# Performance work log

Hardware: AMD Instinct MI355X
Metric: run time of the kernel (lower is better)

## Reference

```python
import jax, jax.numpy as jnp
import numpy as np

MC = 16384
N_STEPS = 120
PERIOD = 30
N_MAT = 4
N_STR = 21
WIDTH_DIFF = 50
WIDTH_VAN = 30
WIDTH_EXO = 20
N_HIDDEN = 3  # n_layers=4 -> input layer + 3 hidden layers + output layer
R = 0.05
TIMEGRID = jnp.asarray(np.linspace(0.0, 1.0, N_STEPS + 1).astype(np.float32))
STRIKES = jnp.asarray(np.linspace(0.8, 1.2, N_STR).astype(np.float32))


def _init_net(key, d_in, width, d_out):
    ks = jax.random.split(key, 6)
    f = lambda k, shape, fan: jax.random.normal(k, shape, jnp.float32) / np.sqrt(fan).astype(np.float32)
    return dict(
        W0=f(ks[0], (N_MAT, d_in, width), d_in),
        b0=f(ks[1], (N_MAT, width), width),
        hW=f(ks[2], (N_MAT, N_HIDDEN, width, width), width),
        hb=f(ks[3], (N_MAT, N_HIDDEN, width), width),
        Wo=f(ks[4], (N_MAT, width, d_out), width),
        bo=f(ks[5], (N_MAT, d_out), width),
    )


def setup_inputs() -> dict:
    key = jax.random.key(0)
    kz, kd, kv, ke = jax.random.split(key, 4)
    inp = {
        "S0": jnp.ones((1,), jnp.float32),
        "z": jax.random.normal(kz, (MC, N_STEPS), jnp.float32),
    }
    for name, net in (("d", _init_net(kd, 2, WIDTH_DIFF, 1)),
                      ("v", _init_net(kv, 2, WIDTH_VAN, N_STR * N_MAT)),
                      ("e", _init_net(ke, N_STEPS + 2, WIDTH_EXO, 1))):
        for pn, arr in net.items():
            inp[name + pn] = arr
    inp["MC_samples"] = MC
    inp["ind_T"] = N_STEPS
    inp["period_length"] = PERIOD
    return inp


def _mlp(x, W0, b0, hW, hb, Wo, bo, softplus_out):
    h = jax.nn.relu(x @ W0 + b0)
    for k in range(hW.shape[0]):  # static small number of hidden layers
        h = jax.nn.relu(h @ hW[k] + hb[k])
    y = h @ Wo + bo
    return jax.nn.softplus(y) if softplus_out else y


def _forward(S0, z, dW0, db0, dhW, dhb, dWo, dbo,
             vW0, vb0, vhW, vhb, vWo, vbo,
             eW0, eb0, ehW, ehb, eWo, ebo,
             MC_samples, ind_T, period_length, remat=False):
    sg = jax.lax.stop_gradient
    S_init = jnp.ones((MC_samples, 1), jnp.float32) * S0
    path0 = jnp.zeros((MC_samples, N_STEPS + 1), jnp.float32).at[:, 0].set(S_init[:, 0])
    zeros_mat = jnp.zeros((N_MAT, N_STR), jnp.float32)

    def step(carry, i):
        S_old, cv_v, cv_e, run_max, path, pv, pvv = carry
        idx = (i - 1) // period_length
        t0 = TIMEGRID[i - 1]
        h = TIMEGRID[i] - TIMEGRID[i - 1]
        sqh = jnp.sqrt(h)
        dWn = sqh * jax.lax.dynamic_slice_in_dim(z, i - 1, 1, 1)  # (MC,1)
        t = jnp.full_like(S_old, t0)
        diff = _mlp(jnp.concatenate([t, S_old], 1),
                    dW0[idx], db0[idx], dhW[idx], dhb[idx], dWo[idx], dbo[idx], True)
        Sd, diffd = sg(S_old), sg(diff)
        S_new = (S_old
                 + R * S_old * h / (1.0 + R * Sd * sqh)
                 + S_old * diff * dWn / (1.0 + Sd * diffd * sqh))
        disc = jnp.exp(-R * t0)
        cv_v = cv_v + disc * Sd * diffd * dWn * _mlp(
            jnp.concatenate([t, Sd], 1),
            vW0[idx], vb0[idx], vhW[idx], vhb[idx], vWo[idx], vbo[idx], False)
        cv_e = cv_e + disc * Sd * diffd * dWn * _mlp(
            jnp.concatenate([t, path], 1),
            eW0[idx], eb0[idx], ehW[idx], ehb[idx], eWo[idx], ebo[idx], False)
        path = jax.lax.dynamic_update_slice(path, sg(S_new), (0, i))
        run_max = jnp.maximum(run_max, S_new)
        # vanilla prices at maturities (i multiple of period_length)
        ind_m = i // period_length - 1
        disc_i = jnp.exp(-R * TIMEGRID[i])
        cv_row = jax.lax.dynamic_slice_in_dim(
            cv_v.reshape(MC_samples, N_MAT, N_STR), ind_m, 1, 1)[:, 0, :]
        pr = disc_i * jnp.maximum(S_new - STRIKES[None, :], 0.0) - cv_row  # (MC, N_STR)
        is_mat = (i % period_length) == 0
        pv = jnp.where(is_mat, jax.lax.dynamic_update_index_in_dim(pv, pr.mean(0), ind_m, 0), pv)
        pvv = jnp.where(is_mat, jax.lax.dynamic_update_index_in_dim(pvv, jnp.var(pr, axis=0, ddof=1), ind_m, 0), pvv)
        return (S_new, cv_v, cv_e, run_max, path, pv, pvv), None

    body = jax.checkpoint(step) if remat else step
    carry0 = (S_init,
              jnp.zeros((MC_samples, N_STR * N_MAT), jnp.float32),
              jnp.zeros((MC_samples, 1), jnp.float32),
              S_init, path0, zeros_mat, zeros_mat)
    (S_T, cv_v, cv_e, run_max, path, pv, pvv), _ = jax.lax.scan(
        body, carry0, jnp.arange(1, ind_T + 1))

    sgv = jax.lax.stop_gradient
    exotic = run_max - S_T
    discT = jnp.exp(-R * TIMEGRID[ind_T])
    e = discT * exotic
    error = sgv(e) - jnp.mean(sgv(e)) - sgv(cv_e)
    price_exo = e - cv_e
    return pv, pvv, price_exo, price_exo.mean(), jnp.var(price_exo, ddof=1), error


def reference(S0, z, dW0, db0, dhW, dhb, dWo, dbo,
              vW0, vb0, vhW, vhb, vWo, vbo,
              eW0, eb0, ehW, ehb, eWo, ebo,
              MC_samples, ind_T, period_length):
    return _forward(S0, z, dW0, db0, dhW, dhb, dWo, dbo,
                    vW0, vb0, vhW, vhb, vWo, vbo,
                    eW0, eb0, ehW, ehb, eWo, ebo,
                    MC_samples, ind_T, period_length)
```

## Files before the change

### kernel.cpp

```cpp
#include <hip/hip_runtime.h>
#include <math.h>

#define MC      16384
#define NSTEPS  120
#define PER     30
#define NMAT    4
#define NSTR    21
#define RRATE   0.05f
#define NBLK    512
#define NSAMP   32

typedef short short8  __attribute__((ext_vector_type(8)));
typedef short short4v __attribute__((ext_vector_type(4)));
typedef float f32x4   __attribute__((ext_vector_type(4)));

#define WS_PRPART 0
#define WS_EPART  (NMAT*NSTR*2*NBLK)
#define WS_MEANE  (WS_EPART + NBLK)

#define OUT_PV    0
#define OUT_PVV   84
#define OUT_PEXO  168
#define OUT_MEAN  16552
#define OUT_VAR   16553
#define OUT_ERR   16554

__device__ __forceinline__ float tgridf(int i)  { return (float)((double)i * (1.0/120.0)); }
__device__ __forceinline__ float strikef(int s) { return (float)(0.8 + (double)s * 0.02); }
__device__ __forceinline__ float softplusf(float x){
  return fmaxf(x, 0.0f) + log1pf(expf(-fabsf(x)));
}
__device__ __forceinline__ unsigned short f2bf(float f){
  unsigned u = __builtin_bit_cast(unsigned, f);
  unsigned r = (u + 0x7FFFu + ((u>>16)&1u)) >> 16;
  return (unsigned short)r;
}
__device__ __forceinline__ float bf2f(unsigned short u){
  return __builtin_bit_cast(float, ((unsigned)u)<<16);
}
__device__ __forceinline__ int swaddr(int row, int slot, int inner){
  return row*256 + (((slot + row) & 15) << 4) + inner;
}
__device__ __forceinline__ short8 rdA(const unsigned short* H, int mt, int base, int lane){
  int addr = swaddr(mt*16 + (lane&15), base + (lane>>4), 0);
  return *(const short8*)((const char*)H + addr);
}
__device__ __forceinline__ f32x4 mm(short8 a, short8 b, f32x4 c){
  return __builtin_amdgcn_mfma_f32_16x16x32_bf16(a, b, c, 0, 0, 0);
}
__device__ __forceinline__ void stD(unsigned short* H, int colbase, int mt, int lane,
                                    f32x4 acc, bool relu){
  int col  = colbase + (lane & 15);
  int slot = col >> 3, inner = (col & 7)*2;
  #pragma unroll
  for (int i2=0;i2<4;++i2){
    int rw = mt*16 + ((lane>>4)<<2) + i2;
    float v = acc[i2];
    if (relu) v = fmaxf(v, 0.0f);
    *(unsigned short*)((char*)H + swaddr(rw, slot, inner)) = f2bf(v);
  }
}
__device__ __forceinline__ short8 mkBd(const float* __restrict__ W, const float* __restrict__ bias,
                                       int n0, int kt, int lane){
  short8 r;
  int n = n0 + (lane&15);
  #pragma unroll
  for (int i2=0;i2<8;++i2){
    int k = kt*32 + ((lane>>4)<<3) + i2;
    float w;
    if (k<50)       w = (n<50)? W[k*50+n] : 0.f;
    else if (k==50) w = (n<50)? bias[n] : ((n==50)? 1.f : 0.f);
    else            w = 0.f;
    r[i2] = (short)f2bf(w);
  }
  return r;
}
__device__ __forceinline__ short8 mkBq(const float* __restrict__ W, const float* __restrict__ bias,
                                       int KV, int n0, int lane){
  short8 r;
  int n = n0 + (lane&15);
  #pragma unroll
  for (int i2=0;i2<8;++i2){
    int k = ((lane>>4)<<3) + i2;
    float w;
    if (k<KV)       w = (n<KV)? W[k*KV+n] : 0.f;
    else if (k==KV) w = (n<KV)? bias[n] : ((n==KV)? 1.f : 0.f);
    else            w = 0.f;
    r[i2] = (short)f2bf(w);
  }
  return r;
}

extern "C" __global__ void __launch_bounds__(256,2) mc_main(
    const float* __restrict__ S0p, const float* __restrict__ z,
    const float* __restrict__ dW0, const float* __restrict__ db0,
    const float* __restrict__ dhW, const float* __restrict__ dhb,
    const float* __restrict__ dWo, const float* __restrict__ dbo,
    const float* __restrict__ vW0, const float* __restrict__ vb0,
    const float* __restrict__ vhW, const float* __restrict__ vhb,
    const float* __restrict__ vWo, const float* __restrict__ vbo,
    const float* __restrict__ eW0, const float* __restrict__ eb0,
    const float* __restrict__ ehW, const float* __restrict__ ehb,
    const float* __restrict__ eWo, const float* __restrict__ ebo,
    float* __restrict__ out, float* __restrict__ ws)
{
  __shared__ unsigned short Hb0[NSAMP*128];
  __shared__ unsigned short Hb1[NSAMP*128];
  __shared__ short8 BqL[4][3][64];
  __shared__ short8 BdL[4][6][64];
  __shared__ float vh3f[NSAMP*40];
  __shared__ float zper[NSAMP*30];
  __shared__ float eW0per[NMAT*600];
  __shared__ float dW0s[128];
  __shared__ float db0s[64];
  __shared__ float vW0s[64];
  __shared__ float vb0s[32];
  __shared__ float eW0ts[20];
  __shared__ float eb0s[20];
  __shared__ float dWoL[64];
  __shared__ float eWoL[32];
  __shared__ float Sb[NSAMP], ebuf[NSAMP];
  __shared__ float part[2*84*2];

  const int tid  = threadIdx.x;
  const int lane = tid & 63;
  const int wid  = __builtin_amdgcn_readfirstlane(tid >> 6);
  const int blk  = blockIdx.x;
  const int r    = tid >> 3;
  const int cc   = tid & 7;

  const int  ntd = wid;
  const bool isv = (wid < 2);
  const int  ntq = wid & 1;

  const float S0v = S0p[0];
  float S = S0v, runmax = S0v, cvE = 0.f;
  f32x4 rr[3];
  #pragma unroll
  for (int q=0;q<3;++q){ rr[q][0]=0.f; rr[q][1]=0.f; rr[q][2]=0.f; rr[q][3]=0.f; }
  float aE[NMAT][4];
  #pragma unroll
  for (int mt2=0;mt2<NMAT;++mt2){ aE[mt2][0]=0.f; aE[mt2][1]=0.f; aE[mt2][2]=0.f; aE[mt2][3]=0.f; }
  float G_[4] = {0.f,0.f,0.f,0.f};

  #pragma unroll 1
  for (int p=0;p<NMAT;++p){
    for (int q=tid; q<NSAMP*30; q+=256){ int r2=q/30, c2=q%30; zper[q] = z[(size_t)(blk*NSAMP+r2)*NSTEPS + p*30 + c2]; }
    for (int q=tid; q<NMAT*600; q+=256){ int mat=q/600, k=q%600; eW0per[q] = eW0[mat*2440 + p*600 + 20 + k]; }
    if (tid < 128){
      int rw = tid>>6, j = tid&63;
      dW0s[tid] = (j<50)? dW0[p*100 + rw*50 + j] : 0.f;
    } else if (tid < 192){
      int j = tid-128;
      db0s[j] = (j<50)? db0[p*50+j] : ((j==50)? 1.f : 0.f);
    } else {
      int idx = tid-192, rw = idx>>5, j = idx&31;
      vW0s[idx] = (j<30)? vW0[p*60 + rw*30 + j] : 0.f;
    }
    if (tid < 32)       vb0s[tid] = (tid<30)? vb0[p*30+tid] : ((tid==30)? 1.f : 0.f);
    else if (tid < 52){ int j=tid-32; eW0ts[j]=eW0[p*2440+j]; eb0s[j]=eb0[p*20+j]; }
    else if (tid < 116){ int j=tid-52; dWoL[j] = (j<50)? dWo[p*50+j] : 0.f; }
    else if (tid < 148){ int j=tid-116; eWoL[j] = (j<20)? eWo[p*20+j] : 0.f; }

    const float dboS = dbo[p], eboS = ebo[p];

    const float* dhWp = dhW + p*7500;
    const float* dhbp = dhb + p*150;
    BdL[wid][0][lane] = mkBd(dhWp,      dhbp,     ntd*16, 0, lane);
    BdL[wid][1][lane] = mkBd(dhWp,      dhbp,     ntd*16, 1, lane);
    BdL[wid][2][lane] = mkBd(dhWp+2500, dhbp+50,  ntd*16, 0, lane);
    BdL[wid][3][lane] = mkBd(dhWp+2500, dhbp+50,  ntd*16, 1, lane);
    BdL[wid][4][lane] = mkBd(dhWp+5000, dhbp+100, ntd*16, 0, lane);
    BdL[wid][5][lane] = mkBd(dhWp+5000, dhbp+100, ntd*16, 1, lane);
    {
      const float* qW    = isv ? (vhW + p*2700) : (ehW + p*1200);
      const float* qb    = isv ? (vhb + p*90)   : (ehb + p*60);
      const int    qstep = isv ? 900 : 400;
      const int    qN    = isv ? 30  : 20;
      BqL[wid][0][lane] = mkBq(qW,         qb,        qN, ntq*16, lane);
      BqL[wid][1][lane] = mkBq(qW+qstep,   qb+qN,     qN, ntq*16, lane);
      BqL[wid][2][lane] = mkBq(qW+2*qstep, qb+2*qN,   qN, ntq*16, lane);
    }
    const int qbase = isv ? 8 : 12;
    const int qcolb = (isv?64:96) + ntq*16;

    __syncthreads();

    #pragma unroll 1
    for (int ii=1; ii<=PER; ++ii){
      const float t0  = tgridf(p*PER + ii - 1);
      const float t1  = tgridf(p*PER + ii);
      const float h   = t1 - t0;
      const float sqh = sqrtf(h);

      {
        short8 hv;
        #pragma unroll
        for (int k=0;k<8;++k){
          int j = cc*8 + k;
          float u = fmaxf(fmaf(t0, dW0s[j], fmaf(S, dW0s[64+j], db0s[j])), 0.f);
          hv[k] = (short)f2bf(u);
        }
        *(short8*)((char*)Hb0 + swaddr(r, cc, 0)) = hv;
        short4v vv;
        #pragma unroll
        for (int k=0;k<4;++k){
          int j = cc*4 + k;
          float u = fmaxf(fmaf(t0, vW0s[j], fmaf(S, vW0s[32+j], vb0s[j])), 0.f);
          vv[k] = (short)f2bf(u);
        }
        *(short4v*)((char*)Hb0 + swaddr(r, 8+(cc>>1), (cc&1)*8)) = vv;
        short4v ev = {0,0,0,0};
        if (cc < 5){
          const int o = (ii-1)*20 + cc*4;
          f32x4 w0 = *(const f32x4*)&eW0per[        o];
          f32x4 w1 = *(const f32x4*)&eW0per[ 600 +  o];
          f32x4 w2 = *(const f32x4*)&eW0per[1200 +  o];
          f32x4 w3 = *(const f32x4*)&eW0per[1800 +  o];
          #pragma unroll
          for (int k=0;k<4;++k){
            aE[0][k] = fmaf(S, w0[k], aE[0][k]);
            aE[1][k] = fmaf(S, w1[k], aE[1][k]);
            aE[2][k] = fmaf(S, w2[k], aE[2][k]);
            aE[3][k] = fmaf(S, w3[k], aE[3][k]);
            float a = (p==0)?aE[0][k]:(p==1)?aE[1][k]:(p==2)?aE[2][k]:aE[3][k];
            int j = cc*4 + k;
            float e0 = fmaxf(t0*eW0ts[j] + a + eb0s[j], 0.f);
            ev[k] = (short)f2bf(e0);
          }
        } else if (cc == 5){
          ev[0] = (short)0x3F80;
        }
        *(short4v*)((char*)Hb0 + swaddr(r, 12+(cc>>1), (cc&1)*8)) = ev;
      }
      __syncthreads();
      {
        short8 b0 = BdL[wid][0][lane], b1 = BdL[wid][1][lane];
        short8 a00=rdA(Hb0,0,0,lane), a01=rdA(Hb0,0,4,lane);
        short8 a10=rdA(Hb0,1,0,lane), a11=rdA(Hb0,1,4,lane);
        f32x4 c0={0.f,0.f,0.f,0.f}, c1={0.f,0.f,0.f,0.f};
        c0=mm(a00,b0,c0); c0=mm(a01,b1,c0);
        c1=mm(a10,b0,c1); c1=mm(a11,b1,c1);
        stD(Hb1, ntd*16, 0, lane, c0, true);
        stD(Hb1, ntd*16, 1, lane, c1, true);
        short8 Bq = BqL[wid][0][lane];
        short8 q0=rdA(Hb0,0,qbase,lane), q1=rdA(Hb0,1,qbase,lane);
        f32x4 cq0={0.f,0.f,0.f,0.f}, cq1={0.f,0.f,0.f,0.f};
        cq0=mm(q0,Bq,cq0); cq1=mm(q1,Bq,cq1);
        stD(Hb1, qcolb, 0, lane, cq0, true);
        stD(Hb1, qcolb, 1, lane, cq1, true);
      }
      __syncthreads();
      {
        short8 b0 = BdL[wid][2][lane], b1 = BdL[wid][3][lane];
        short8 a00=rdA(Hb1,0,0,lane), a01=rdA(Hb1,0,4,lane);
        short8 a10=rdA(Hb1,1,0,lane), a11=rdA(Hb1,1,4,lane);
        f32x4 c0={0.f,0.f,0.f,0.f}, c1={0.f,0.f,0.f,0.f};
        c0=mm(a00,b0,c0); c0=mm(a01,b1,c0);
        c1=mm(a10,b0,c1); c1=mm(a11,b1,c1);
        stD(Hb0, ntd*16, 0, lane, c0, true);
        stD(Hb0, ntd*16, 1, lane, c1, true);
        short8 Bq = BqL[wid][1][lane];
        short8 q0=rdA(Hb1,0,qbase,lane), q1=rdA(Hb1,1,qbase,lane);
        f32x4 cq0={0.f,0.f,0.f,0.f}, cq1={0.f,0.f,0.f,0.f};
        cq0=mm(q0,Bq,cq0); cq1=mm(q1,Bq,cq1);
        stD(Hb0, qcolb, 0, lane, cq0, true);
        stD(Hb0, qcolb, 1, lane, cq1, true);
      }
      __syncthreads();
      {
        short8 b0 = BdL[wid][4][lane], b1 = BdL[wid][5][lane];
        short8 a00=rdA(Hb0,0,0,lane), a01=rdA(Hb0,0,4,lane);
        short8 a10=rdA(Hb0,1,0,lane), a11=rdA(Hb0,1,4,lane);
        f32x4 c0={0.f,0.f,0.f,0.f}, c1={0.f,0.f,0.f,0.f};
        c0=mm(a00,b0,c0); c0=mm(a01,b1,c0);
        c1=mm(a10,b0,c1); c1=mm(a11,b1,c1);
        stD(Hb1, ntd*16, 0, lane, c0, true);
        stD(Hb1, ntd*16, 1, lane, c1, true);
        short8 Bq = BqL[wid][2][lane];
        short8 q0=rdA(Hb0,0,qbase,lane), q1=rdA(Hb0,1,qbase,lane);
        f32x4 cq0={0.f,0.f,0.f,0.f}, cq1={0.f,0.f,0.f,0.f};
        cq0=mm(q0,Bq,cq0); cq1=mm(q1,Bq,cq1);
        if (isv){
          #pragma unroll
          for (int i2=0;i2<4;++i2){
            int r0 = ((lane>>4)<<2) + i2;
            vh3f[ r0     *40 + ntq*16 + (lane&15)] = fmaxf(cq0[i2], 0.f);
            vh3f[(16+r0) *40 + ntq*16 + (lane&15)] = fmaxf(cq1[i2], 0.f);
          }
        } else {
          stD(Hb1, qcolb, 0, lane, cq0, true);
          stD(Hb1, qcolb, 1, lane, cq1, true);
        }
      }
      __syncthreads();
      {
        float yp = 0.f;
        {
          short8 hv = *(const short8*)((const char*)Hb1 + swaddr(r, cc, 0));
          #pragma unroll
          for (int k=0;k<8;++k) yp = fmaf(bf2f((unsigned short)hv[k]), dWoL[cc*8+k], yp);
        }
        float yep = 0.f;
        if (cc < 5){
          short4v hv = *(const short4v*)((const char*)Hb1 + swaddr(r, 12+(cc>>1), (cc&1)*8));
          #pragma unroll
          for (int k=0;k<4;++k) yep = fmaf(bf2f((unsigned short)hv[k]), eWoL[cc*4+k], yep);
        }
        #pragma unroll
        for (int mk=1; mk<8; mk<<=1){ yp += __shfl_xor(yp, mk); yep += __shfl_xor(yep, mk); }
        const float y    = yp + dboS;
        const float diff = softplusf(y);
        const float zv   = zper[r*30 + (ii-1)];
        const float dWn  = sqh * zv;
        const float d1 = 1.f + RRATE*S*sqh;
        const float d2 = 1.f + S*diff*sqh;
        const float Snew = S + RRATE*S*h/d1 + S*diff*dWn/d2;
        const float disc = expf(-RRATE*t0);
        const float coef = disc * S * diff * dWn;
        cvE = fmaf(coef, yep + eboS, cvE);
        runmax = fmaxf(runmax, Snew);
        {
          f32x4 vv = *(const f32x4*)&vh3f[r*40 + cc*4];
          #pragma unroll
          for (int k=0;k<4;++k) G_[k] = fmaf(coef, vv[k], G_[k]);
        }
        S = Snew;

        if (ii==PER){
          short4v gv;
          #pragma unroll
          for (int k=0;k<4;++k){ gv[k] = (short)f2bf(G_[k]); G_[k] = 0.f; }
          *(short4v*)((char*)Hb0 + swaddr(r, cc>>1, (cc&1)*8)) = gv;
          if (cc==0) Sb[r] = S;
        }
      }

      if (ii==PER){
        __syncthreads();
        const float disc_i = expf(-RRATE*t1);
        const float* vWop = vWo + p*2520;
        const float* vbop = vbo + p*84;
        #pragma unroll
        for (int q3=0;q3<3;++q3){
          const int T = wid*3 + q3;
          const int mtr = T/6, ntr = T%6;
          short8 a = rdA(Hb0, mtr, 0, lane);
          const int col = ntr*16 + (lane&15);
          short8 bw;
          #pragma unroll
          for (int i2=0;i2<8;++i2){
            int k = ((lane>>4)<<3)+i2;
            float w = 0.f;
            if (col < 84){
              if (k < 30)       w = vWop[k*84+col];
              else if (k == 30) w = vbop[col];
            }
            bw[i2] = (short)f2bf(w);
          }
          f32x4 d4 = {0.f,0.f,0.f,0.f};
          d4 = mm(a,bw,d4);
          const int s = col - p*NSTR;
          const bool inr = (s>=0) && (s<NSTR) && (col<84);
          const float K = strikef(s);
          float ssum=0.f, ssq=0.f;
          #pragma unroll
          for (int i2=0;i2<4;++i2){
            int row = mtr*16 + ((lane>>4)<<2) + i2;
            rr[q3][i2] += d4[i2];
            if (inr){
              float pr = disc_i*fmaxf(Sb[row]-K,0.f) - rr[q3][i2];
              ssum += pr; ssq = fmaf(pr,pr,ssq);
            }
          }
          ssum += __shfl_down(ssum,16); ssum += __shfl_down(ssum,32);
          ssq  += __shfl_down(ssq ,16); ssq  += __shfl_down(ssq ,32);
          if (inr && lane<16){
            part[(mtr*84+col)*2+0] = ssum;
            part[(mtr*84+col)*2+1] = ssq;
          }
        }
        __syncthreads();
        if (tid < NSTR){
          int cidx = p*NSTR + tid;
          ws[WS_PRPART + (cidx*2+0)*NBLK + blk] = part[cidx*2] + part[(84+cidx)*2];
        } else if (tid >= 64 && tid < 64+NSTR){
          int cidx = p*NSTR + (tid-64);
          ws[WS_PRPART + (cidx*2+1)*NBLK + blk] = part[cidx*2+1] + part[(84+cidx)*2+1];
        }
        __syncthreads();
      }
    }
  }

  if (cc==0){
    const float discT = expf(-RRATE);
    const float e = discT * (runmax - S);
    out[OUT_PEXO + blk*NSAMP + r] = e - cvE;
    ebuf[r] = e;
  }
  __syncthreads();
  if (tid < 32){
    float se = ebuf[tid];
    se += __shfl_down(se,16); se += __shfl_down(se,8);
    se += __shfl_down(se,4);  se += __shfl_down(se,2); se += __shfl_down(se,1);
    if (tid==0) ws[WS_EPART + blk] = se;
  }
}

extern "C" __global__ void fin_pv(const float* __restrict__ ws, float* __restrict__ out){
  const int t = threadIdx.x;
  if (t >= NMAT*NSTR) return;
  float sum=0.0f, ssq=0.0f;
  for (int b=0;b<NBLK;++b){
    sum += ws[WS_PRPART + (t*2+0)*NBLK + b];
    ssq += ws[WS_PRPART + (t*2+1)*NBLK + b];
  }
  out[OUT_PV  + t] = sum * (1.0f/MC);
  out[OUT_PVV + t] = (ssq - sum*sum*(1.0f/MC)) * (1.0f/(MC-1));
}

extern "C" __global__ void fin_pe(float* out, float* ws){
  __shared__ float sA[4], sB[4], sC[4];
  const int t = threadIdx.x;
  float sum=0.0f, ssq=0.0f;
  for (int idx=t; idx<MC; idx+=256){
    const float v = out[OUT_PEXO+idx];
    sum += v; ssq = fmaf(v,v,ssq);
  }
  float es = ws[WS_EPART + t] + ws[WS_EPART + 256 + t];
  for (int o=32;o>0;o>>=1){
    sum += __shfl_down(sum,o);
    ssq += __shfl_down(ssq,o);
    es  += __shfl_down(es,o);
  }
  const int w=t>>6, lane=t&63;
  if (lane==0){ sA[w]=sum; sB[w]=ssq; sC[w]=es; }
  __syncthreads();
  if (t==0){
    const float s=sA[0]+sA[1]+sA[2]+sA[3];
    const float q=sB[0]+sB[1]+sB[2]+sB[3];
    const float e=sC[0]+sC[1]+sC[2]+sC[3];
    out[OUT_MEAN]=s*(1.0f/MC);
    out[OUT_VAR]=(q - s*s*(1.0f/MC))*(1.0f/(MC-1));
    ws[WS_MEANE]=e*(1.0f/MC);
  }
}

extern "C" __global__ void fin_err(float* out, const float* __restrict__ ws){
  const int m = blockIdx.x*blockDim.x + threadIdx.x;
  if (m < MC) out[OUT_ERR+m] = out[OUT_PEXO+m] - ws[WS_MEANE];
}

extern "C" void kernel_launch(void* const* d_in, const int* in_sizes, int n_in,
                              void* d_out, int out_size, void* d_ws, size_t ws_size,
                              hipStream_t stream){
  (void)in_sizes; (void)n_in; (void)out_size; (void)ws_size;
  const float* S0 =(const float*)d_in[0];
  const float* z  =(const float*)d_in[1];
  const float* dW0=(const float*)d_in[2];
  const float* db0=(const float*)d_in[3];
  const float* dhW=(const float*)d_in[4];
  const float* dhb=(const float*)d_in[5];
  const float* dWo=(const float*)d_in[6];
  const float* dbo=(const float*)d_in[7];
  const float* vW0=(const float*)d_in[8];
  const float* vb0=(const float*)d_in[9];
  const float* vhW=(const float*)d_in[10];
  const float* vhb=(const float*)d_in[11];
  const float* vWo=(const float*)d_in[12];
  const float* vbo=(const float*)d_in[13];
  const float* eW0=(const float*)d_in[14];
  const float* eb0=(const float*)d_in[15];
  const float* ehW=(const float*)d_in[16];
  const float* ehb=(const float*)d_in[17];
  const float* eWo=(const float*)d_in[18];
  const float* ebo=(const float*)d_in[19];
  float* out=(float*)d_out;
  float* ws =(float*)d_ws;

  mc_main<<<dim3(NBLK),dim3(256),0,stream>>>(S0,z,dW0,db0,dhW,dhb,dWo,dbo,
                                             vW0,vb0,vhW,vhb,vWo,vbo,
                                             eW0,eb0,ehW,ehb,eWo,ebo,out,ws);
  fin_pv <<<dim3(1), dim3(128),0,stream>>>(ws,out);
  fin_pe <<<dim3(1), dim3(256),0,stream>>>(out,ws);
  fin_err<<<dim3(64),dim3(256),0,stream>>>(out,ws);
}
```

Before: 467.7 us.

## Give each wavefront its own 8-sample tile to eliminate per-layer block barriers

Result: slower. 587.3 us (+25.6%).

```diff
diff --git a/kernel.cpp b/kernel.cpp
--- a/kernel.cpp
+++ b/kernel.cpp
@@ -16,7 +16,7 @@
 
 #define WS_PRPART 0
 #define WS_EPART  (NMAT*NSTR*2*NBLK)
-#define WS_MEANE  (WS_EPART + NBLK)
+#define WS_MEANE  (WS_EPART + 2048)
 
 #define OUT_PV    0
 #define OUT_PVV   84
@@ -89,6 +89,34 @@
     r[i2] = (short)f2bf(w);
   }
   return r;
+}
+__device__ __forceinline__ void layer_all(const unsigned short* src, unsigned short* dst,
+                                          const short8 (*__restrict__ Bd)[64],
+                                          const short8 (*__restrict__ Bv)[64],
+                                          const short8 (*__restrict__ Be)[64],
+                                          int l, int lane){
+  short8 a0 = rdA(src,0,0,lane), a1 = rdA(src,0,4,lane);
+  short8 av = rdA(src,0,8,lane);
+  short8 ae = rdA(src,0,12,lane);
+  #pragma unroll
+  for (int nt=0;nt<4;++nt){
+    f32x4 c={0.f,0.f,0.f,0.f};
+    c = mm(a0, Bd[l*8+nt*2  ][lane], c);
+    c = mm(a1, Bd[l*8+nt*2+1][lane], c);
+    stD(dst, nt*16, 0, lane, c, true);
+  }
+  #pragma unroll
+  for (int nt=0;nt<2;++nt){
+    f32x4 c={0.f,0.f,0.f,0.f};
+    c = mm(av, Bv[l*2+nt][lane], c);
+    stD(dst, 64+nt*16, 0, lane, c, true);
+  }
+  #pragma unroll
+  for (int nt=0;nt<2;++nt){
+    f32x4 c={0.f,0.f,0.f,0.f};
+    c = mm(ae, Be[l*2+nt][lane], c);
+    stD(dst, 96+nt*16, 0, lane, c, true);
+  }
 }
 
 extern "C" __global__ void __launch_bounds__(256,2) mc_main(
@@ -104,87 +132,70 @@
     const float* __restrict__ eWo, const float* __restrict__ ebo,
     float* __restrict__ out, float* __restrict__ ws)
 {
-  __shared__ unsigned short Hb0[NSAMP*128];
-  __shared__ unsigned short Hb1[NSAMP*128];
-  __shared__ short8 BqL[4][3][64];
-  __shared__ short8 BdL[4][6][64];
-  __shared__ float vh3f[NSAMP*40];
+  __shared__ unsigned short tiles[4][2][2048];
+  __shared__ short8 BdA[24][64];
+  __shared__ short8 BvA[6][64];
+  __shared__ short8 BeA[6][64];
+  __shared__ unsigned short eW0b[2400];
   __shared__ float zper[NSAMP*30];
-  __shared__ float eW0per[NMAT*600];
-  __shared__ float dW0s[128];
-  __shared__ float db0s[64];
-  __shared__ float vW0s[64];
-  __shared__ float vb0s[32];
-  __shared__ float eW0ts[20];
-  __shared__ float eb0s[20];
-  __shared__ float dWoL[64];
-  __shared__ float eWoL[32];
-  __shared__ float Sb[NSAMP], ebuf[NSAMP];
-  __shared__ float part[2*84*2];
+  __shared__ float dW0s[128], db0s[64], vW0s[64], vb0s[32];
+  __shared__ float eW0ts[20], eb0s[20], dWoL[64], eWoL[32];
+  __shared__ float SbW[32];
 
   const int tid  = threadIdx.x;
   const int lane = tid & 63;
   const int wid  = __builtin_amdgcn_readfirstlane(tid >> 6);
   const int blk  = blockIdx.x;
-  const int r    = tid >> 3;
-  const int cc   = tid & 7;
-
-  const int  ntd = wid;
-  const bool isv = (wid < 2);
-  const int  ntq = wid & 1;
+  const int s    = lane >> 3;
+  const int c8   = lane & 7;
+
+  unsigned short* T0 = &tiles[wid][0][0];
+  unsigned short* T1 = &tiles[wid][1][0];
+
+  for (int q=tid; q<4*2*2048; q+=256) ((unsigned short*)tiles)[q] = 0;
 
   const float S0v = S0p[0];
   float S = S0v, runmax = S0v, cvE = 0.f;
-  f32x4 rr[3];
-  #pragma unroll
-  for (int q=0;q<3;++q){ rr[q][0]=0.f; rr[q][1]=0.f; rr[q][2]=0.f; rr[q][3]=0.f; }
   float aE[NMAT][4];
   #pragma unroll
-  for (int mt2=0;mt2<NMAT;++mt2){ aE[mt2][0]=0.f; aE[mt2][1]=0.f; aE[mt2][2]=0.f; aE[mt2][3]=0.f; }
+  for (int m2=0;m2<NMAT;++m2){ aE[m2][0]=0.f; aE[m2][1]=0.f; aE[m2][2]=0.f; aE[m2][3]=0.f; }
   float G_[4] = {0.f,0.f,0.f,0.f};
+  f32x4 rr[6];
+  #pragma unroll
+  for (int q=0;q<6;++q){ rr[q][0]=0.f; rr[q][1]=0.f; rr[q][2]=0.f; rr[q][3]=0.f; }
 
   #pragma unroll 1
   for (int p=0;p<NMAT;++p){
+    __syncthreads();
     for (int q=tid; q<NSAMP*30; q+=256){ int r2=q/30, c2=q%30; zper[q] = z[(size_t)(blk*NSAMP+r2)*NSTEPS + p*30 + c2]; }
-    for (int q=tid; q<NMAT*600; q+=256){ int mat=q/600, k=q%600; eW0per[q] = eW0[mat*2440 + p*600 + 20 + k]; }
-    if (tid < 128){
-      int rw = tid>>6, j = tid&63;
-      dW0s[tid] = (j<50)? dW0[p*100 + rw*50 + j] : 0.f;
-    } else if (tid < 192){
-      int j = tid-128;
-      db0s[j] = (j<50)? db0[p*50+j] : ((j==50)? 1.f : 0.f);
-    } else {
-      int idx = tid-192, rw = idx>>5, j = idx&31;
-      vW0s[idx] = (j<30)? vW0[p*60 + rw*30 + j] : 0.f;
-    }
+    for (int q=tid; q<2400; q+=256){ int mat=q/600, k=q%600; eW0b[q] = f2bf(eW0[mat*2440 + p*600 + 20 + k]); }
+    if (tid < 128){ int rw=tid>>6, j=tid&63; dW0s[tid] = (j<50)? dW0[p*100+rw*50+j] : 0.f; }
+    else if (tid < 192){ int j=tid-128; db0s[j] = (j<50)? db0[p*50+j] : ((j==50)? 1.f : 0.f); }
+    else { int idx=tid-192, rw=idx>>5, j=idx&31; vW0s[idx] = (j<30)? vW0[p*60+rw*30+j] : 0.f; }
     if (tid < 32)       vb0s[tid] = (tid<30)? vb0[p*30+tid] : ((tid==30)? 1.f : 0.f);
     else if (tid < 52){ int j=tid-32; eW0ts[j]=eW0[p*2440+j]; eb0s[j]=eb0[p*20+j]; }
     else if (tid < 116){ int j=tid-52; dWoL[j] = (j<50)? dWo[p*50+j] : 0.f; }
     else if (tid < 148){ int j=tid-116; eWoL[j] = (j<20)? eWo[p*20+j] : 0.f; }
+    {
+      const float* dhWp = dhW + p*7500; const float* dhbp = dhb + p*150;
+      const float* vhWp = vhW + p*2700; const float* vhbp = vhb + p*90;
+      const float* ehWp = ehW + p*1200; const float* ehbp = ehb + p*60;
+      for (int fid = wid; fid < 36; fid += 4){
+        if (fid < 24){
+          int l = fid>>3, nt = (fid>>1)&3, kt = fid&1;
+          BdA[fid][lane] = mkBd(dhWp + l*2500, dhbp + l*50, nt*16, kt, lane);
+        } else if (fid < 30){
+          int q = fid-24, l = q>>1, nt = q&1;
+          BvA[q][lane] = mkBq(vhWp + l*900, vhbp + l*30, 30, nt*16, lane);
+        } else {
+          int q = fid-30, l = q>>1, nt = q&1;
+          BeA[q][lane] = mkBq(ehWp + l*400, ehbp + l*20, 20, nt*16, lane);
+        }
+      }
+    }
+    __syncthreads();
 
     const float dboS = dbo[p], eboS = ebo[p];
-
-    const float* dhWp = dhW + p*7500;
-    const float* dhbp = dhb + p*150;
-    BdL[wid][0][lane] = mkBd(dhWp,      dhbp,     ntd*16, 0, lane);
-    BdL[wid][1][lane] = mkBd(dhWp,      dhbp,     ntd*16, 1, lane);
-    BdL[wid][2][lane] = mkBd(dhWp+2500, dhbp+50,  ntd*16, 0, lane);
-    BdL[wid][3][lane] = mkBd(dhWp+2500, dhbp+50,  ntd*16, 1, lane);
-    BdL[wid][4][lane] = mkBd(dhWp+5000, dhbp+100, ntd*16, 0, lane);
-    BdL[wid][5][lane] = mkBd(dhWp+5000, dhbp+100, ntd*16, 1, lane);
-    {
-      const float* qW    = isv ? (vhW + p*2700) : (ehW + p*1200);
-      const float* qb    = isv ? (vhb + p*90)   : (ehb + p*60);
-      const int    qstep = isv ? 900 : 400;
-      const int    qN    = isv ? 30  : 20;
-      BqL[wid][0][lane] = mkBq(qW,         qb,        qN, ntq*16, lane);
-      BqL[wid][1][lane] = mkBq(qW+qstep,   qb+qN,     qN, ntq*16, lane);
-      BqL[wid][2][lane] = mkBq(qW+2*qstep, qb+2*qN,   qN, ntq*16, lane);
-    }
-    const int qbase = isv ? 8 : 12;
-    const int qcolb = (isv?64:96) + ntq*16;
-
-    __syncthreads();
 
     #pragma unroll 1
     for (int ii=1; ii<=PER; ++ii){
@@ -197,121 +208,63 @@
         short8 hv;
         #pragma unroll
         for (int k=0;k<8;++k){
-          int j = cc*8 + k;
+          int j = c8*8 + k;
           float u = fmaxf(fmaf(t0, dW0s[j], fmaf(S, dW0s[64+j], db0s[j])), 0.f);
           hv[k] = (short)f2bf(u);
         }
-        *(short8*)((char*)Hb0 + swaddr(r, cc, 0)) = hv;
+        *(short8*)((char*)T0 + swaddr(s, c8, 0)) = hv;
         short4v vv;
         #pragma unroll
         for (int k=0;k<4;++k){
-          int j = cc*4 + k;
+          int j = c8*4 + k;
           float u = fmaxf(fmaf(t0, vW0s[j], fmaf(S, vW0s[32+j], vb0s[j])), 0.f);
           vv[k] = (short)f2bf(u);
         }
-        *(short4v*)((char*)Hb0 + swaddr(r, 8+(cc>>1), (cc&1)*8)) = vv;
+        *(short4v*)((char*)T0 + swaddr(s, 8+(c8>>1), (c8&1)*8)) = vv;
         short4v ev = {0,0,0,0};
-        if (cc < 5){
-          const int o = (ii-1)*20 + cc*4;
-          f32x4 w0 = *(const f32x4*)&eW0per[        o];
-          f32x4 w1 = *(const f32x4*)&eW0per[ 600 +  o];
-          f32x4 w2 = *(const f32x4*)&eW0per[1200 +  o];
-          f32x4 w3 = *(const f32x4*)&eW0per[1800 +  o];
+        if (c8 < 5){
+          const int o = (ii-1)*20 + c8*4;
           #pragma unroll
           for (int k=0;k<4;++k){
-            aE[0][k] = fmaf(S, w0[k], aE[0][k]);
-            aE[1][k] = fmaf(S, w1[k], aE[1][k]);
-            aE[2][k] = fmaf(S, w2[k], aE[2][k]);
-            aE[3][k] = fmaf(S, w3[k], aE[3][k]);
+            float w0 = bf2f(eW0b[      o+k]);
+            float w1 = bf2f(eW0b[ 600+ o+k]);
+            float w2 = bf2f(eW0b[1200+ o+k]);
+            float w3 = bf2f(eW0b[1800+ o+k]);
+            aE[0][k] = fmaf(S, w0, aE[0][k]);
+            aE[1][k] = fmaf(S, w1, aE[1][k]);
+            aE[2][k] = fmaf(S, w2, aE[2][k]);
+            aE[3][k] = fmaf(S, w3, aE[3][k]);
             float a = (p==0)?aE[0][k]:(p==1)?aE[1][k]:(p==2)?aE[2][k]:aE[3][k];
-            int j = cc*4 + k;
+            int j = c8*4 + k;
             float e0 = fmaxf(t0*eW0ts[j] + a + eb0s[j], 0.f);
             ev[k] = (short)f2bf(e0);
           }
-        } else if (cc == 5){
+        } else if (c8 == 5){
           ev[0] = (short)0x3F80;
         }
-        *(short4v*)((char*)Hb0 + swaddr(r, 12+(cc>>1), (cc&1)*8)) = ev;
+        *(short4v*)((char*)T0 + swaddr(s, 12+(c8>>1), (c8&1)*8)) = ev;
       }
-      __syncthreads();
-      {
-        short8 b0 = BdL[wid][0][lane], b1 = BdL[wid][1][lane];
-        short8 a00=rdA(Hb0,0,0,lane), a01=rdA(Hb0,0,4,lane);
-        short8 a10=rdA(Hb0,1,0,lane), a11=rdA(Hb0,1,4,lane);
-        f32x4 c0={0.f,0.f,0.f,0.f}, c1={0.f,0.f,0.f,0.f};
-        c0=mm(a00,b0,c0); c0=mm(a01,b1,c0);
-        c1=mm(a10,b0,c1); c1=mm(a11,b1,c1);
-        stD(Hb1, ntd*16, 0, lane, c0, true);
-        stD(Hb1, ntd*16, 1, lane, c1, true);
-        short8 Bq = BqL[wid][0][lane];
-        short8 q0=rdA(Hb0,0,qbase,lane), q1=rdA(Hb0,1,qbase,lane);
-        f32x4 cq0={0.f,0.f,0.f,0.f}, cq1={0.f,0.f,0.f,0.f};
-        cq0=mm(q0,Bq,cq0); cq1=mm(q1,Bq,cq1);
-        stD(Hb1, qcolb, 0, lane, cq0, true);
-        stD(Hb1, qcolb, 1, lane, cq1, true);
-      }
-      __syncthreads();
-      {
-        short8 b0 = BdL[wid][2][lane], b1 = BdL[wid][3][lane];
-        short8 a00=rdA(Hb1,0,0,lane), a01=rdA(Hb1,0,4,lane);
-        short8 a10=rdA(Hb1,1,0,lane), a11=rdA(Hb1,1,4,lane);
-        f32x4 c0={0.f,0.f,0.f,0.f}, c1={0.f,0.f,0.f,0.f};
-        c0=mm(a00,b0,c0); c0=mm(a01,b1,c0);
-        c1=mm(a10,b0,c1); c1=mm(a11,b1,c1);
-        stD(Hb0, ntd*16, 0, lane, c0, true);
-        stD(Hb0, ntd*16, 1, lane, c1, true);
-        short8 Bq = BqL[wid][1][lane];
-        short8 q0=rdA(Hb1,0,qbase,lane), q1=rdA(Hb1,1,qbase,lane);
-        f32x4 cq0={0.f,0.f,0.f,0.f}, cq1={0.f,0.f,0.f,0.f};
-        cq0=mm(q0,Bq,cq0); cq1=mm(q1,Bq,cq1);
-        stD(Hb0, qcolb, 0, lane, cq0, true);
-        stD(Hb0, qcolb, 1, lane, cq1, true);
-      }
-      __syncthreads();
-      {
-        short8 b0 = BdL[wid][4][lane], b1 = BdL[wid][5][lane];
-        short8 a00=rdA(Hb0,0,0,lane), a01=rdA(Hb0,0,4,lane);
-        short8 a10=rdA(Hb0,1,0,lane), a11=rdA(Hb0,1,4,lane);
-        f32x4 c0={0.f,0.f,0.f,0.f}, c1={0.f,0.f,0.f,0.f};
-        c0=mm(a00,b0,c0); c0=mm(a01,b1,c0);
-        c1=mm(a10,b0,c1); c1=mm(a11,b1,c1);
-        stD(Hb1, ntd*16, 0, lane, c0, true);
-        stD(Hb1, ntd*16, 1, lane, c1, true);
-        short8 Bq = BqL[wid][2][lane];
-        short8 q0=rdA(Hb0,0,qbase,lane), q1=rdA(Hb0,1,qbase,lane);
-        f32x4 cq0={0.f,0.f,0.f,0.f}, cq1={0.f,0.f,0.f,0.f};
-        cq0=mm(q0,Bq,cq0); cq1=mm(q1,Bq,cq1);
-        if (isv){
-          #pragma unroll
-          for (int i2=0;i2<4;++i2){
-            int r0 = ((lane>>4)<<2) + i2;
-            vh3f[ r0     *40 + ntq*16 + (lane&15)] = fmaxf(cq0[i2], 0.f);
-            vh3f[(16+r0) *40 + ntq*16 + (lane&15)] = fmaxf(cq1[i2], 0.f);
-          }
-        } else {
-          stD(Hb1, qcolb, 0, lane, cq0, true);
-          stD(Hb1, qcolb, 1, lane, cq1, true);
-        }
-      }
-      __syncthreads();
+      layer_all(T0, T1, BdA, BvA, BeA, 0, lane);
+      layer_all(T1, T0, BdA, BvA, BeA, 1, lane);
+      layer_all(T0, T1, BdA, BvA, BeA, 2, lane);
       {
         float yp = 0.f;
         {
-          short8 hv = *(const short8*)((const char*)Hb1 + swaddr(r, cc, 0));
-          #pragma unroll
-          for (int k=0;k<8;++k) yp = fmaf(bf2f((unsigned short)hv[k]), dWoL[cc*8+k], yp);
+          short8 hv = *(const short8*)((const char*)T1 + swaddr(s, c8, 0));
+          #pragma unroll
+          for (int k=0;k<8;++k) yp = fmaf(bf2f((unsigned short)hv[k]), dWoL[c8*8+k], yp);
         }
         float yep = 0.f;
-        if (cc < 5){
-          short4v hv = *(const short4v*)((const char*)Hb1 + swaddr(r, 12+(cc>>1), (cc&1)*8));
-          #pragma unroll
-          for (int k=0;k<4;++k) yep = fmaf(bf2f((unsigned short)hv[k]), eWoL[cc*4+k], yep);
+        {
+          short4v hv = *(const short4v*)((const char*)T1 + swaddr(s, 12+(c8>>1), (c8&1)*8));
+          #pragma unroll
+          for (int k=0;k<4;++k) yep = fmaf(bf2f((unsigned short)hv[k]), eWoL[c8*4+k], yep);
         }
         #pragma unroll
         for (int mk=1; mk<8; mk<<=1){ yp += __shfl_xor(yp, mk); yep += __shfl_xor(yep, mk); }
         const float y    = yp + dboS;
         const float diff = softplusf(y);
-        const float zv   = zper[r*30 + (ii-1)];
+        const float zv   = zper[(wid*8+s)*30 + (ii-1)];
         const float dWn  = sqh * zv;
         const float d1 = 1.f + RRATE*S*sqh;
         const float d2 = 1.f + S*diff*sqh;
@@ -321,9 +274,9 @@
         cvE = fmaf(coef, yep + eboS, cvE);
         runmax = fmaxf(runmax, Snew);
         {
-          f32x4 vv = *(const f32x4*)&vh3f[r*40 + cc*4];
-          #pragma unroll
-          for (int k=0;k<4;++k) G_[k] = fmaf(coef, vv[k], G_[k]);
+          short4v hv = *(const short4v*)((const char*)T1 + swaddr(s, 8+(c8>>1), (c8&1)*8));
+          #pragma unroll
+          for (int k=0;k<4;++k) G_[k] = fmaf(coef, bf2f((unsigned short)hv[k]), G_[k]);
         }
         S = Snew;
 
@@ -331,22 +284,20 @@
           short4v gv;
           #pragma unroll
           for (int k=0;k<4;++k){ gv[k] = (short)f2bf(G_[k]); G_[k] = 0.f; }
-          *(short4v*)((char*)Hb0 + swaddr(r, cc>>1, (cc&1)*8)) = gv;
-          if (cc==0) Sb[r] = S;
+          *(short4v*)((char*)T0 + swaddr(s, c8>>1, (c8&1)*8)) = gv;
+          if (c8==0) SbW[wid*8+s] = S;
         }
       }
 
       if (ii==PER){
-        __syncthreads();
+        short8 a = rdA(T0, 0, 0, lane);
         const float disc_i = expf(-RRATE*t1);
         const float* vWop = vWo + p*2520;
         const float* vbop = vbo + p*84;
+        float* pw = (float*)T1;
         #pragma unroll
-        for (int q3=0;q3<3;++q3){
-          const int T = wid*3 + q3;
-          const int mtr = T/6, ntr = T%6;
-          short8 a = rdA(Hb0, mtr, 0, lane);
-          const int col = ntr*16 + (lane&15);
+        for (int nt=0;nt<6;++nt){
+          const int col = nt*16 + (lane&15);
           short8 bw;
           #pragma unroll
           for (int i2=0;i2<8;++i2){
@@ -360,51 +311,46 @@
           }
           f32x4 d4 = {0.f,0.f,0.f,0.f};
           d4 = mm(a,bw,d4);
-          const int s = col - p*NSTR;
-          const bool inr = (s>=0) && (s<NSTR) && (col<84);
-          const float K = strikef(s);
+          const int st = col - p*NSTR;
+          const bool inr = (st>=0) && (st<NSTR) && (col<84);
+          const float K = strikef(st);
           float ssum=0.f, ssq=0.f;
           #pragma unroll
           for (int i2=0;i2<4;++i2){
-            int row = mtr*16 + ((lane>>4)<<2) + i2;
-            rr[q3][i2] += d4[i2];
-            if (inr){
-              float pr = disc_i*fmaxf(Sb[row]-K,0.f) - rr[q3][i2];
+            int row = ((lane>>4)<<2) + i2;
+            rr[nt][i2] += d4[i2];
+            if (row < 8 && inr){
+              float pr = disc_i*fmaxf(SbW[wid*8+row]-K,0.f) - rr[nt][i2];
               ssum += pr; ssq = fmaf(pr,pr,ssq);
             }
           }
-          ssum += __shfl_down(ssum,16); ssum += __shfl_down(ssum,32);
-          ssq  += __shfl_down(ssq ,16); ssq  += __shfl_down(ssq ,32);
-          if (inr && lane<16){
-            part[(mtr*84+col)*2+0] = ssum;
-            part[(mtr*84+col)*2+1] = ssq;
-          }
+          ssum += __shfl_down(ssum,16);
+          ssq  += __shfl_down(ssq ,16);
+          if (inr && lane<16){ pw[st*2] = ssum; pw[st*2+1] = ssq; }
         }
         __syncthreads();
         if (tid < NSTR){
-          int cidx = p*NSTR + tid;
-          ws[WS_PRPART + (cidx*2+0)*NBLK + blk] = part[cidx*2] + part[(84+cidx)*2];
+          float v = 0.f;
+          #pragma unroll
+          for (int w2=0;w2<4;++w2) v += ((const float*)&tiles[w2][1][0])[tid*2];
+          ws[WS_PRPART + ((p*NSTR+tid)*2+0)*NBLK + blk] = v;
         } else if (tid >= 64 && tid < 64+NSTR){
-          int cidx = p*NSTR + (tid-64);
-          ws[WS_PRPART + (cidx*2+1)*NBLK + blk] = part[cidx*2+1] + part[(84+cidx)*2+1];
-        }
-        __syncthreads();
+          int j = tid-64; float v = 0.f;
+          #pragma unroll
+          for (int w2=0;w2<4;++w2) v += ((const float*)&tiles[w2][1][0])[j*2+1];
+          ws[WS_PRPART + ((p*NSTR+j)*2+1)*NBLK + blk] = v;
+        }
       }
     }
   }
 
-  if (cc==0){
+  {
     const float discT = expf(-RRATE);
     const float e = discT * (runmax - S);
-    out[OUT_PEXO + blk*NSAMP + r] = e - cvE;
-    ebuf[r] = e;
-  }
-  __syncthreads();
-  if (tid < 32){
-    float se = ebuf[tid];
-    se += __shfl_down(se,16); se += __shfl_down(se,8);
-    se += __shfl_down(se,4);  se += __shfl_down(se,2); se += __shfl_down(se,1);
-    if (tid==0) ws[WS_EPART + blk] = se;
+    if (c8==0) out[OUT_PEXO + blk*NSAMP + wid*8 + s] = e - cvE;
+    float se = (c8==0)? e : 0.f;
+    se += __shfl_down(se,32); se += __shfl_down(se,16); se += __shfl_down(se,8);
+    if (lane==0) ws[WS_EPART + blk*4 + wid] = se;
   }
 }
 
@@ -428,7 +374,8 @@
     const float v = out[OUT_PEXO+idx];
     sum += v; ssq = fmaf(v,v,ssq);
   }
-  float es = ws[WS_EPART + t] + ws[WS_EPART + 256 + t];
+  float es = 0.0f;
+  for (int idx=t; idx<2048; idx+=256) es += ws[WS_EPART + idx];
   for (int o=32;o>0;o>>=1){
     sum += __shfl_down(sum,o);
     ssq += __shfl_down(ssq,o);
```
